# Kernel optimization log

Hardware: AMD Instinct MI355X
Metric: run time of the kernel (lower is better)

Reference implementation:

```python
import jax, jax.numpy as jnp
import numpy as np

HIDDEN = 2048
NUM_HEADS = 16
HEAD_DIM = 128
BLOCK_SIZE = 64
NUM_ACTIVE_BLOCKS = 4  # diagonal pattern -> bandwidth = 2 blocks each side
NEG_INF = -1e30  # stand-in for -inf that is safe under softmax in fp32


def _block_diagonal_additive_mask(seq_len: int) -> jnp.ndarray:
    """Token-level additive mask [S, S]; 0 where block |bi-bj|<=bandwidth, -inf else."""
    bandwidth = NUM_ACTIVE_BLOCKS // 2
    bid = jnp.arange(seq_len) // BLOCK_SIZE  # [S]
    active = jnp.abs(bid[:, None] - bid[None, :]) <= bandwidth  # [S, S] bool
    return jnp.where(active, 0.0, NEG_INF).astype(jnp.float32)


def setup_inputs() -> dict:
    key = jax.random.key(0)
    k0, k1, k2, k3, k4 = jax.random.split(key, 5)
    B, S = 2, 2048
    scale = 1.0 / np.sqrt(HIDDEN)
    return {
        "hidden_states": jax.random.normal(k0, (B, S, HIDDEN), dtype=jnp.float32),
        "Wq": jax.random.normal(k1, (HIDDEN, NUM_HEADS * HEAD_DIM), dtype=jnp.float32) * scale,
        "Wk": jax.random.normal(k2, (HIDDEN, NUM_HEADS * HEAD_DIM), dtype=jnp.float32) * scale,
        "Wv": jax.random.normal(k3, (HIDDEN, NUM_HEADS * HEAD_DIM), dtype=jnp.float32) * scale,
        "Wo": jax.random.normal(k4, (NUM_HEADS * HEAD_DIM, HIDDEN), dtype=jnp.float32) * scale,
    }


def reference(hidden_states, Wq, Wk, Wv, Wo):
    B, S, _ = hidden_states.shape
    scaling = HEAD_DIM ** -0.5

    # projections -> [B, H, S, D]
    def split_heads(x):
        return x.reshape(B, S, NUM_HEADS, HEAD_DIM).transpose(0, 2, 1, 3)

    q = split_heads(hidden_states @ Wq)
    k = split_heads(hidden_states @ Wk)
    v = split_heads(hidden_states @ Wv)

    mask = _block_diagonal_additive_mask(S)  # [S, S]

    # scores [B, H, S, S]
    scores = jnp.einsum("bhsd,bhtd->bhst", q, k) * scaling + mask[None, None]
    attn = jax.nn.softmax(scores.astype(jnp.float32), axis=-1).astype(q.dtype)

    out = jnp.einsum("bhst,bhtd->bhsd", attn, v)  # [B, H, S, D]
    out = out.transpose(0, 2, 1, 3).reshape(B, S, NUM_HEADS * HEAD_DIM)
    return out @ Wo
```

## Files before the change

kernel.cpp:

```cpp
#include <hip/hip_runtime.h>

typedef __attribute__((ext_vector_type(4))) float f32x4;
typedef __attribute__((ext_vector_type(16))) float f32x16;
typedef __attribute__((ext_vector_type(8))) _Float16 f16x8;
typedef __attribute__((ext_vector_type(4))) _Float16 f16x4;

__device__ __forceinline__ void gload_lds16(const void* g, void* l) {
  __builtin_amdgcn_global_load_lds((__attribute__((address_space(1))) void*)(g),
                                   (__attribute__((address_space(3))) void*)(l), 16, 0, 0);
}

#define BAR() asm volatile("s_barrier" ::: "memory")
#define WAITV6() asm volatile("s_waitcnt vmcnt(6)" ::: "memory")
#define WAITV0() asm volatile("s_waitcnt vmcnt(0)" ::: "memory")

__global__ __launch_bounds__(256) void prep(const float* __restrict__ Hs,
                                            const float* __restrict__ W0, const float* __restrict__ W1,
                                            const float* __restrict__ W2, const float* __restrict__ W3,
                                            _Float16* __restrict__ Hb, _Float16* __restrict__ Wt) {
  __shared__ _Float16 tile[64][65];
  const int bid = blockIdx.x, tid = threadIdx.x;
  if (bid < 8192) {
    int i = (bid * 256 + tid) * 4;
    float4 v = *(const float4*)(Hs + i);
    f16x4 o = { (_Float16)v.x, (_Float16)v.y, (_Float16)v.z, (_Float16)v.w };
    *(f16x4*)(Hb + i) = o;
    return;
  }
  const int t = bid - 8192;
  const int z = t >> 10, k0 = ((t >> 5) & 31) * 64, n0 = (t & 31) * 64;
  const float* W = z == 0 ? W0 : z == 1 ? W1 : z == 2 ? W2 : W3;
  _Float16* Wo_ = Wt + (size_t)z * (2048u * 2048u);
  #pragma unroll
  for (int p = 0; p < 4; ++p) {
    int o = p * 256 + tid, r = o >> 4, c = o & 15;
    float4 v = *(const float4*)(W + (size_t)(k0 + r) * 2048 + n0 + c * 4);
    tile[r][c * 4 + 0] = (_Float16)v.x;
    tile[r][c * 4 + 1] = (_Float16)v.y;
    tile[r][c * 4 + 2] = (_Float16)v.z;
    tile[r][c * 4 + 3] = (_Float16)v.w;
  }
  __syncthreads();
  #pragma unroll
  for (int p = 0; p < 2; ++p) {
    int o = p * 256 + tid, nl = o >> 3, c = o & 7;
    f16x8 u;
    #pragma unroll
    for (int i = 0; i < 8; ++i) u[i] = tile[c * 8 + i][nl];
    *(f16x8*)(Wo_ + (size_t)(n0 + nl) * 2048 + k0 + c * 8) = u;
  }
}

template <int SM, int SN, typename OutT>
__device__ __forceinline__ void gemm_tile(const _Float16* __restrict__ A,
                                          const _Float16* __restrict__ Bt,
                                          OutT* __restrict__ C,
                                          int K, int N, int m0, int n0, _Float16* S) {
  _Float16* As = S;
  _Float16* Bs = S + SM * 64 * 64;
  const int tid = threadIdx.x;
  const int lane = tid & 63, w = tid >> 6, l32 = lane & 31, half = lane >> 5;
  const int wm = (w & 1) * SM * 32, wn = (w >> 1) * SN * 32;
  f32x16 acc[SM][SN];
  #pragma unroll
  for (int s = 0; s < SM; ++s)
    #pragma unroll
    for (int t = 0; t < SN; ++t) acc[s][t] = 0;

  for (int k0 = 0; k0 < K; k0 += 64) {
    __syncthreads();
    #pragma unroll
    for (int p = 0; p < SM * 2; ++p) {
      int o = p * 256 + tid, r = o >> 3, c = o & 7;
      gload_lds16(A + (size_t)(m0 + r) * K + k0 + ((c ^ (r & 7)) * 8), (char*)As + o * 16);
    }
    #pragma unroll
    for (int p = 0; p < SN * 2; ++p) {
      int o = p * 256 + tid, r = o >> 3, c = o & 7;
      gload_lds16(Bt + (size_t)(n0 + r) * K + k0 + ((c ^ (r & 7)) * 8), (char*)Bs + o * 16);
    }
    __builtin_amdgcn_s_waitcnt(0);
    __syncthreads();
    #pragma unroll
    for (int kk = 0; kk < 4; ++kk) {
      const int slot = ((2 * kk + half) ^ (l32 & 7)) * 8;
      f16x8 af[SM], bf[SN];
      #pragma unroll
      for (int s = 0; s < SM; ++s) af[s] = *(const f16x8*)(As + (wm + s * 32 + l32) * 64 + slot);
      #pragma unroll
      for (int t = 0; t < SN; ++t) bf[t] = *(const f16x8*)(Bs + (wn + t * 32 + l32) * 64 + slot);
      #pragma unroll
      for (int s = 0; s < SM; ++s)
        #pragma unroll
        for (int t = 0; t < SN; ++t)
          acc[s][t] = __builtin_amdgcn_mfma_f32_32x32x16_f16(bf[t], af[s], acc[s][t], 0, 0, 0);
    }
  }
  #pragma unroll
  for (int s = 0; s < SM; ++s) {
    const size_t row = (size_t)(m0 + wm + s * 32 + l32);
    #pragma unroll
    for (int t = 0; t < SN; ++t) {
      #pragma unroll
      for (int g = 0; g < 4; ++g) {
        const int col = n0 + wn + t * 32 + g * 8 + 4 * half;
        if constexpr (sizeof(OutT) == 2) {
          f16x4 o = { (_Float16)acc[s][t][4 * g + 0], (_Float16)acc[s][t][4 * g + 1],
                      (_Float16)acc[s][t][4 * g + 2], (_Float16)acc[s][t][4 * g + 3] };
          *(f16x4*)((_Float16*)C + row * N + col) = o;
        } else {
          f32x4 o = { acc[s][t][4 * g + 0], acc[s][t][4 * g + 1],
                      acc[s][t][4 * g + 2], acc[s][t][4 * g + 3] };
          *(f32x4*)((float*)C + row * N + col) = o;
        }
      }
    }
  }
}

__device__ __forceinline__ void gemm256(const _Float16* __restrict__ A,
                                        const _Float16* __restrict__ Bt,
                                        _Float16* __restrict__ C, int ldc,
                                        int m0, int n0, _Float16* S) {
  _Float16* const As0 = S;
  _Float16* const As1 = S + 16384;
  _Float16* const Bs0 = S + 32768;
  _Float16* const Bs1 = S + 49152;
  const int tid = (int)threadIdx.x;
  const int lane = tid & 63, w = tid >> 6, l32 = lane & 31, half = lane >> 5;
  const int wm = (w & 1) * 128, wn = (w >> 1) * 64;

  f32x16 acc[4][2];
  #pragma unroll
  for (int s = 0; s < 4; ++s)
    #pragma unroll
    for (int t = 0; t < 2; ++t) acc[s][t] = 0;

  f16x8 af[2][4];
  f16x8 bf[2][4];

  auto stageA = [&](_Float16* dst, int ar, int kt) {
    const int r = tid >> 3, c = tid & 7;
    gload_lds16(A + (size_t)(m0 + ar + r) * 2048 + kt * 64 + ((c ^ (r & 7)) << 3),
                (char*)dst + ar * 128 + tid * 16);
  };
  auto stageB = [&](_Float16* dst, int br, int kt) {
    const int r = tid >> 3, c = tid & 7;
    gload_lds16(Bt + (size_t)(n0 + br + r) * 2048 + kt * 64 + ((c ^ (r & 7)) << 3),
                (char*)dst + br * 128 + tid * 16);
  };
  auto ldA = [&](const _Float16* as, int p) {
    #pragma unroll
    for (int s2 = 0; s2 < 2; ++s2)
      #pragma unroll
      for (int kk = 0; kk < 4; ++kk)
        af[s2][kk] = *(const f16x8*)(as + (wm + p * 64 + s2 * 32 + l32) * 64 +
                                     (((2 * kk + half) ^ (l32 & 7)) << 3));
  };
  auto ldB = [&](const _Float16* bs, int q) {
    #pragma unroll
    for (int kk = 0; kk < 4; ++kk)
      bf[q][kk] = *(const f16x8*)(bs + (wn + q * 32 + l32) * 64 +
                                  (((2 * kk + half) ^ (l32 & 7)) << 3));
  };
  auto mm8 = [&](int sp, int q) {
    __builtin_amdgcn_s_setprio(1);
    #pragma unroll
    for (int kk = 0; kk < 4; ++kk)
      #pragma unroll
      for (int s2 = 0; s2 < 2; ++s2)
        acc[sp * 2 + s2][q] = __builtin_amdgcn_mfma_f32_32x32x16_f16(
            bf[q][kk], af[s2][kk], acc[sp * 2 + s2][q], 0, 0, 0);
    __builtin_amdgcn_s_setprio(0);
  };

  stageA(As0, 0, 0); stageA(As0, 64, 0); stageA(As0, 128, 0); stageA(As0, 192, 0);
  stageB(Bs0, 0, 0); stageB(Bs0, 64, 0); stageB(Bs0, 128, 0); stageB(Bs0, 192, 0);
  stageA(As1, 0, 1); stageA(As1, 128, 1);
  stageB(Bs1, 0, 1); stageB(Bs1, 64, 1); stageB(Bs1, 128, 1); stageB(Bs1, 192, 1);
  WAITV6();
  BAR();

  auto tile = [&](int kt, _Float16* Ac, _Float16* Bc, _Float16* An) {
    const bool g1 = (kt + 1) < 32, g2 = (kt + 2) < 32;
    ldA(Ac, 0);
    ldB(Bc, 0); ldB(Bc, 1);
    if (g1) { stageA(An, 64, kt + 1); stageA(An, 192, kt + 1); }
    mm8(0, 0);
    BAR();
    if (g2) { stageA(Ac, 0, kt + 2); stageA(Ac, 128, kt + 2); }
    mm8(0, 1);
    BAR();
    ldA(Ac, 1);
    if (g2) { stageB(Bc, 0, kt + 2); stageB(Bc, 64, kt + 2);
              stageB(Bc, 128, kt + 2); stageB(Bc, 192, kt + 2); }
    mm8(1, 1);
    mm8(1, 0);
    if (g2) { WAITV6(); } else { WAITV0(); }
    BAR();
  };

  #pragma unroll 1
  for (int kt = 0; kt < 32; kt += 2) {
    tile(kt, As0, Bs0, As1);
    tile(kt + 1, As1, Bs1, As0);
  }

  #pragma unroll
  for (int s = 0; s < 4; ++s) {
    const size_t row = (size_t)(wm + s * 32 + l32);
    #pragma unroll
    for (int t = 0; t < 2; ++t)
      #pragma unroll
      for (int g = 0; g < 4; ++g) {
        const int col = wn + t * 32 + g * 8 + 4 * half;
        f16x4 o = { (_Float16)acc[s][t][4 * g + 0], (_Float16)acc[s][t][4 * g + 1],
                    (_Float16)acc[s][t][4 * g + 2], (_Float16)acc[s][t][4 * g + 3] };
        *(f16x4*)(C + row * ldc + col) = o;
      }
  }
}

__device__ __forceinline__ void gemm128(const _Float16* __restrict__ A,
                                        const _Float16* __restrict__ Bt,
                                        _Float16* __restrict__ C, int ldc,
                                        int m0, int n0, _Float16* S) {
  _Float16* const As0 = S;
  _Float16* const As1 = S + 8192;
  _Float16* const Bs0 = S + 16384;
  _Float16* const Bs1 = S + 32768;
  const int tid = (int)threadIdx.x;
  const int lane = tid & 63, w = tid >> 6, l32 = lane & 31, half = lane >> 5;
  const int wm = (w & 1) * 64, wn = (w >> 1) * 64;

  f32x16 acc[2][2];
  #pragma unroll
  for (int s = 0; s < 2; ++s)
    #pragma unroll
    for (int t = 0; t < 2; ++t) acc[s][t] = 0;

  f16x8 af[2][4], bf[2][4];

  auto stA = [&](_Float16* dst, int ar, int kt) {
    const int r = tid >> 3, c = tid & 7;
    gload_lds16(A + (size_t)(m0 + ar + r) * 2048 + kt * 64 + ((c ^ (r & 7)) << 3),
                (char*)dst + ar * 128 + tid * 16);
  };
  auto stB = [&](_Float16* dst, int br, int kt) {
    const int r = tid >> 3, c = tid & 7;
    gload_lds16(Bt + (size_t)(n0 + br + r) * 2048 + kt * 64 + ((c ^ (r & 7)) << 3),
                (char*)dst + br * 128 + tid * 16);
  };
  auto ldA_ = [&](const _Float16* as) {
    #pragma unroll
    for (int s2 = 0; s2 < 2; ++s2)
      #pragma unroll
      for (int kk = 0; kk < 4; ++kk)
        af[s2][kk] = *(const f16x8*)(as + (wm + s2 * 32 + l32) * 64 +
                                     (((2 * kk + half) ^ (l32 & 7)) << 3));
  };
  auto ldB_ = [&](const _Float16* bs, int q) {
    #pragma unroll
    for (int kk = 0; kk < 4; ++kk)
      bf[q][kk] = *(const f16x8*)(bs + (wn + q * 32 + l32) * 64 +
                                  (((2 * kk + half) ^ (l32 & 7)) << 3));
  };
  auto mmq = [&](int q) {
    __builtin_amdgcn_s_setprio(1);
    #pragma unroll
    for (int kk = 0; kk < 4; ++kk)
      #pragma unroll
      for (int s2 = 0; s2 < 2; ++s2)
        acc[s2][q] = __builtin_amdgcn_mfma_f32_32x32x16_f16(
            bf[q][kk], af[s2][kk], acc[s2][q], 0, 0, 0);
    __builtin_amdgcn_s_setprio(0);
  };

  stA(As0, 0, 0); stA(As0, 64, 0);
  stB(Bs0, 0, 0); stB(Bs0, 64, 0); stB(Bs0, 128, 0); stB(Bs0, 192, 0);
  stA(As1, 0, 1); stA(As1, 64, 1);
  stB(Bs1, 0, 1); stB(Bs1, 64, 1); stB(Bs1, 128, 1); stB(Bs1, 192, 1);
  WAITV6();
  BAR();

  auto tile = [&](int kt, _Float16* Ac, _Float16* Bc) {
    const bool g2 = (kt + 2) < 32;
    ldA_(Ac); ldB_(Bc, 0); ldB_(Bc, 1);
    mmq(0);
    mmq(1);
    BAR();
    if (g2) {
      stA(Ac, 0, kt + 2); stA(Ac, 64, kt + 2);
      stB(Bc, 0, kt + 2); stB(Bc, 64, kt + 2); stB(Bc, 128, kt + 2); stB(Bc, 192, kt + 2);
      WAITV6();
    } else {
      WAITV0();
    }
    BAR();
  };

  #pragma unroll 1
  for (int kt = 0; kt < 32; kt += 2) {
    tile(kt, As0, Bs0);
    tile(kt + 1, As1, Bs1);
  }

  #pragma unroll
  for (int s = 0; s < 2; ++s) {
    const size_t row = (size_t)(wm + s * 32 + l32);
    #pragma unroll
    for (int t = 0; t < 2; ++t)
      #pragma unroll
      for (int g = 0; g < 4; ++g) {
        const int col = wn + t * 32 + g * 8 + 4 * half;
        f16x4 o = { (_Float16)acc[s][t][4 * g + 0], (_Float16)acc[s][t][4 * g + 1],
                    (_Float16)acc[s][t][4 * g + 2], (_Float16)acc[s][t][4 * g + 3] };
        *(f16x4*)(C + row * ldc + col) = o;
      }
  }
}

__global__ __launch_bounds__(512, 2) void qkvv3(const _Float16* __restrict__ Hb,
                                                const _Float16* __restrict__ Wt,
                                                _Float16* __restrict__ Qb,
                                                _Float16* __restrict__ Kb,
                                                _Float16* __restrict__ Vtb) {
  __shared__ _Float16 S[65536];
  const int id = blockIdx.x;
  {
    const int m0 = (id >> 4) * 256, n0 = (id & 15) * 256;
    _Float16* Cq = (n0 < 2048 ? Qb + n0 : Kb + (n0 - 2048)) + (size_t)m0 * 2048;
    gemm256(Hb, Wt, Cq, 2048, m0, n0, S);
  }
  WAITV0();
  BAR();
  {
    const int m0 = (id >> 4) * 128, n0 = (id & 15) * 256;
    gemm128(Wt + (size_t)2 * 4194304, Hb, Vtb + (size_t)m0 * 4096 + n0, 4096, m0, n0, S);
  }
}

__global__ __launch_bounds__(256) void gemm_wo(const _Float16* __restrict__ A,
                                               const _Float16* __restrict__ Bt,
                                               float* __restrict__ C) {
  __shared__ _Float16 S[16384];
  const int t = blockIdx.x;
  gemm_tile<2, 2>(A, Bt, C, 2048, 2048, (t >> 4) * 128, (t & 15) * 128, S);
}

__global__ __launch_bounds__(256) void attn(const _Float16* __restrict__ Qg,
                                            const _Float16* __restrict__ Kg,
                                            const _Float16* __restrict__ Vtg,
                                            _Float16* __restrict__ Og) {
  const int t = blockIdx.x, h = blockIdx.y, b = blockIdx.z;
  __shared__ _Float16 Qs[128 * 128];
  __shared__ _Float16 Ks[64 * 128];
  __shared__ _Float16 Vs[128 * 64];
  const int tid = threadIdx.x;
  const int lane = tid & 63, w = tid >> 6, l16 = lane & 15, quad = lane >> 4;
  const int qbw = 2 * t + (w >> 1);
  const char* QsB = (const char*)Qs;
  const char* KsB = (const char*)Ks;
  const char* VsB = (const char*)Vs;

  #pragma unroll
  for (int p = 0; p < 8; ++p) {
    int o = p * 256 + tid, r = o >> 4, c = o & 15;
    gload_lds16(Qg + (size_t)(b * 2048 + t * 128 + r) * 2048 + h * 128 + ((c ^ (r & 15)) * 8),
                (char*)Qs + o * 16);
  }
  __builtin_amdgcn_s_waitcnt(0);
  __syncthreads();
  f16x8 qf[2][4];
  #pragma unroll
  for (int qc = 0; qc < 2; ++qc)
    #pragma unroll
    for (int ks = 0; ks < 4; ++ks)
      qf[qc][ks] = *(const f16x8*)(QsB + (w * 32 + qc * 16 + l16) * 256 +
                                   (((ks * 4 + quad) ^ l16) * 16));

  const float scale = 0.08838834764831845f;
  float m_[2] = {-1e30f, -1e30f}, l_[2] = {0.f, 0.f};
  f32x4 oacc[8][2];
  #pragma unroll
  for (int dt = 0; dt < 8; ++dt)
    #pragma unroll
    for (int qc = 0; qc < 2; ++qc) oacc[dt][qc] = (f32x4){0.f, 0.f, 0.f, 0.f};

  for (int jj = 0; jj < 6; ++jj) {
    const int j = 2 * t - 2 + jj;
    const int jc = j < 0 ? 0 : (j > 31 ? 31 : j);
    __syncthreads();
    #pragma unroll
    for (int p = 0; p < 4; ++p) {
      int o = p * 256 + tid, r = o >> 4, c = o & 15;
      gload_lds16(Kg + (size_t)(b * 2048 + jc * 64 + r) * 2048 + h * 128 + ((c ^ (r & 15)) * 8),
                  (char*)Ks + o * 16);
    }
    #pragma unroll
    for (int p = 0; p < 4; ++p) {
      int o = p * 256 + tid, d = o >> 3, c = o & 7;
      gload_lds16(Vtg + (size_t)(h * 128 + d) * 4096 + b * 2048 + jc * 64 + ((c ^ (d & 7)) * 8),
                  (char*)Vs + o * 16);
    }
    __builtin_amdgcn_s_waitcnt(0);
    __syncthreads();

    const bool valid = (j >= 0) && (j <= 31) && (j >= qbw - 2) && (j <= qbw + 2);
    if (valid) {
      f32x4 sc[4][2];
      #pragma unroll
      for (int kt = 0; kt < 4; ++kt)
        #pragma unroll
        for (int qc = 0; qc < 2; ++qc) sc[kt][qc] = (f32x4){0.f, 0.f, 0.f, 0.f};
      #pragma unroll
      for (int kt = 0; kt < 4; ++kt)
        #pragma unroll
        for (int ks = 0; ks < 4; ++ks) {
          f16x8 kf = *(const f16x8*)(KsB + (kt * 16 + l16) * 256 + (((ks * 4 + quad) ^ l16) * 16));
          #pragma unroll
          for (int qc = 0; qc < 2; ++qc)
            sc[kt][qc] = __builtin_amdgcn_mfma_f32_16x16x32_f16(kf, qf[qc][ks], sc[kt][qc], 0, 0, 0);
        }
      #pragma unroll
      for (int qc = 0; qc < 2; ++qc) {
        float mj = -1e30f;
        #pragma unroll
        for (int kt = 0; kt < 4; ++kt)
          #pragma unroll
          for (int r = 0; r < 4; ++r) {
            float v = sc[kt][qc][r] * scale;
            sc[kt][qc][r] = v;
            mj = fmaxf(mj, v);
          }
        mj = fmaxf(mj, __shfl_xor(mj, 16));
        mj = fmaxf(mj, __shfl_xor(mj, 32));
        const float mn = fmaxf(m_[qc], mj);
        const float alpha = __expf(m_[qc] - mn);
        float s_ = 0.f;
        #pragma unroll
        for (int kt = 0; kt < 4; ++kt)
          #pragma unroll
          for (int r = 0; r < 4; ++r) {
            float p = __expf(sc[kt][qc][r] - mn);
            sc[kt][qc][r] = p;
            s_ += p;
          }
        s_ += __shfl_xor(s_, 16);
        s_ += __shfl_xor(s_, 32);
        l_[qc] = l_[qc] * alpha + s_;
        m_[qc] = mn;
        #pragma unroll
        for (int dt = 0; dt < 8; ++dt) oacc[dt][qc] *= alpha;
      }
      #pragma unroll
      for (int kt = 0; kt < 4; ++kt) {
        f16x4 pb[2];
        #pragma unroll
        for (int qc = 0; qc < 2; ++qc)
          pb[qc] = (f16x4){ (_Float16)sc[kt][qc][0], (_Float16)sc[kt][qc][1],
                            (_Float16)sc[kt][qc][2], (_Float16)sc[kt][qc][3] };
        #pragma unroll
        for (int dt = 0; dt < 8; ++dt) {
          f16x4 vv = *(const f16x4*)(VsB + (dt * 16 + l16) * 128 +
                                     (((2 * kt + (quad >> 1)) ^ (l16 & 7)) * 16) + (quad & 1) * 8);
          #pragma unroll
          for (int qc = 0; qc < 2; ++qc)
            oacc[dt][qc] = __builtin_amdgcn_mfma_f32_16x16x16f16(vv, pb[qc], oacc[dt][qc], 0, 0, 0);
        }
      }
    }
  }

  #pragma unroll
  for (int qc = 0; qc < 2; ++qc) {
    const float pinv = 1.0f / l_[qc];
    const size_t orow = (size_t)(b * 2048 + t * 128 + w * 32 + qc * 16 + l16);
    #pragma unroll
    for (int dt = 0; dt < 8; ++dt) {
      f16x4 ov = { (_Float16)(oacc[dt][qc][0] * pinv), (_Float16)(oacc[dt][qc][1] * pinv),
                   (_Float16)(oacc[dt][qc][2] * pinv), (_Float16)(oacc[dt][qc][3] * pinv) };
      *(f16x4*)(Og + orow * 2048 + h * 128 + dt * 16 + quad * 4) = ov;
    }
  }
}

extern "C" void kernel_launch(void* const* d_in, const int* in_sizes, int n_in,
                              void* d_out, int out_size, void* d_ws, size_t ws_size,
                              hipStream_t stream) {
  const float* Hs = (const float*)d_in[0];
  const float* Wq = (const float*)d_in[1];
  const float* Wk = (const float*)d_in[2];
  const float* Wv = (const float*)d_in[3];
  const float* Wo = (const float*)d_in[4];
  _Float16* Hb  = (_Float16*)d_ws;
  _Float16* Wt  = Hb  + 8388608;
  _Float16* Qb  = Wt  + 16777216;
  _Float16* Kb  = Qb  + 8388608;
  _Float16* Vtb = Kb  + 8388608;
  _Float16* Ob  = Vtb + 8388608;
  float* out = (float*)d_out;

  prep<<<12288, 256, 0, stream>>>(Hs, Wq, Wk, Wv, Wo, Hb, Wt);
  qkvv3<<<256, 512, 0, stream>>>(Hb, Wt, Qb, Kb, Vtb);
  attn<<<dim3(16, 16, 2), 256, 0, stream>>>(Qb, Kb, Vtb, Ob);
  gemm_wo<<<512, 256, 0, stream>>>(Ob, Wt + (size_t)3 * 4194304, out);
}
```

Measured before the change: 341.0 us.

## Software-pipeline LDS fragment loads in GEMMs and reuse pipelined gemm128 for Wo

Restructures the gemm256 and gemm128 main loops so that register fragments for the next K tile are read from LDS right after the barrier while MFMAs on the current tile proceed. This double-buffers the fragments in registers, which adds register pressure in exchange. The gemm256 loop now stages whole A/B tiles per iteration with adjusted vmcnt waits. The output projection kernel drops the simple unpipelined gemm_tile and uses the templated pipelined gemm128 with 512 threads and 256 blocks, writing float output.

```diff
diff --git a/kernel.cpp b/kernel.cpp
--- a/kernel.cpp
+++ b/kernel.cpp
@@ -11,6 +11,8 @@
 }
 
 #define BAR() asm volatile("s_barrier" ::: "memory")
+#define LGKM0() asm volatile("s_waitcnt lgkmcnt(0)" ::: "memory")
+#define WAITV8() asm volatile("s_waitcnt vmcnt(8)" ::: "memory")
 #define WAITV6() asm volatile("s_waitcnt vmcnt(6)" ::: "memory")
 #define WAITV0() asm volatile("s_waitcnt vmcnt(0)" ::: "memory")
 
@@ -51,73 +53,6 @@
   }
 }
 
-template <int SM, int SN, typename OutT>
-__device__ __forceinline__ void gemm_tile(const _Float16* __restrict__ A,
-                                          const _Float16* __restrict__ Bt,
-                                          OutT* __restrict__ C,
-                                          int K, int N, int m0, int n0, _Float16* S) {
-  _Float16* As = S;
-  _Float16* Bs = S + SM * 64 * 64;
-  const int tid = threadIdx.x;
-  const int lane = tid & 63, w = tid >> 6, l32 = lane & 31, half = lane >> 5;
-  const int wm = (w & 1) * SM * 32, wn = (w >> 1) * SN * 32;
-  f32x16 acc[SM][SN];
-  #pragma unroll
-  for (int s = 0; s < SM; ++s)
-    #pragma unroll
-    for (int t = 0; t < SN; ++t) acc[s][t] = 0;
-
-  for (int k0 = 0; k0 < K; k0 += 64) {
-    __syncthreads();
-    #pragma unroll
-    for (int p = 0; p < SM * 2; ++p) {
-      int o = p * 256 + tid, r = o >> 3, c = o & 7;
-      gload_lds16(A + (size_t)(m0 + r) * K + k0 + ((c ^ (r & 7)) * 8), (char*)As + o * 16);
-    }
-    #pragma unroll
-    for (int p = 0; p < SN * 2; ++p) {
-      int o = p * 256 + tid, r = o >> 3, c = o & 7;
-      gload_lds16(Bt + (size_t)(n0 + r) * K + k0 + ((c ^ (r & 7)) * 8), (char*)Bs + o * 16);
-    }
-    __builtin_amdgcn_s_waitcnt(0);
-    __syncthreads();
-    #pragma unroll
-    for (int kk = 0; kk < 4; ++kk) {
-      const int slot = ((2 * kk + half) ^ (l32 & 7)) * 8;
-      f16x8 af[SM], bf[SN];
-      #pragma unroll
-      for (int s = 0; s < SM; ++s) af[s] = *(const f16x8*)(As + (wm + s * 32 + l32) * 64 + slot);
-      #pragma unroll
-      for (int t = 0; t < SN; ++t) bf[t] = *(const f16x8*)(Bs + (wn + t * 32 + l32) * 64 + slot);
-      #pragma unroll
-      for (int s = 0; s < SM; ++s)
-        #pragma unroll
-        for (int t = 0; t < SN; ++t)
-          acc[s][t] = __builtin_amdgcn_mfma_f32_32x32x16_f16(bf[t], af[s], acc[s][t], 0, 0, 0);
-    }
-  }
-  #pragma unroll
-  for (int s = 0; s < SM; ++s) {
-    const size_t row = (size_t)(m0 + wm + s * 32 + l32);
-    #pragma unroll
-    for (int t = 0; t < SN; ++t) {
-      #pragma unroll
-      for (int g = 0; g < 4; ++g) {
-        const int col = n0 + wn + t * 32 + g * 8 + 4 * half;
-        if constexpr (sizeof(OutT) == 2) {
-          f16x4 o = { (_Float16)acc[s][t][4 * g + 0], (_Float16)acc[s][t][4 * g + 1],
-                      (_Float16)acc[s][t][4 * g + 2], (_Float16)acc[s][t][4 * g + 3] };
-          *(f16x4*)((_Float16*)C + row * N + col) = o;
-        } else {
-          f32x4 o = { acc[s][t][4 * g + 0], acc[s][t][4 * g + 1],
-                      acc[s][t][4 * g + 2], acc[s][t][4 * g + 3] };
-          *(f32x4*)((float*)C + row * N + col) = o;
-        }
-      }
-    }
-  }
-}
-
 __device__ __forceinline__ void gemm256(const _Float16* __restrict__ A,
                                         const _Float16* __restrict__ Bt,
                                         _Float16* __restrict__ C, int ldc,
@@ -136,8 +71,7 @@
     #pragma unroll
     for (int t = 0; t < 2; ++t) acc[s][t] = 0;
 
-  f16x8 af[2][4];
-  f16x8 bf[2][4];
+  f16x8 fA0[2][4], fA1[2][4], fB0[4], fB1[4];
 
   auto stageA = [&](_Float16* dst, int ar, int kt) {
     const int r = tid >> 3, c = tid & 7;
@@ -149,62 +83,68 @@
     gload_lds16(Bt + (size_t)(n0 + br + r) * 2048 + kt * 64 + ((c ^ (r & 7)) << 3),
                 (char*)dst + br * 128 + tid * 16);
   };
-  auto ldA = [&](const _Float16* as, int p) {
+  auto ldA = [&](const _Float16* as, int p, f16x8 (&dst)[2][4]) {
     #pragma unroll
     for (int s2 = 0; s2 < 2; ++s2)
       #pragma unroll
       for (int kk = 0; kk < 4; ++kk)
-        af[s2][kk] = *(const f16x8*)(as + (wm + p * 64 + s2 * 32 + l32) * 64 +
-                                     (((2 * kk + half) ^ (l32 & 7)) << 3));
-  };
-  auto ldB = [&](const _Float16* bs, int q) {
+        dst[s2][kk] = *(const f16x8*)(as + (wm + p * 64 + s2 * 32 + l32) * 64 +
+                                      (((2 * kk + half) ^ (l32 & 7)) << 3));
+  };
+  auto ldB = [&](const _Float16* bs, int q, f16x8 (&dst)[4]) {
     #pragma unroll
     for (int kk = 0; kk < 4; ++kk)
-      bf[q][kk] = *(const f16x8*)(bs + (wn + q * 32 + l32) * 64 +
-                                  (((2 * kk + half) ^ (l32 & 7)) << 3));
-  };
-  auto mm8 = [&](int sp, int q) {
+      dst[kk] = *(const f16x8*)(bs + (wn + q * 32 + l32) * 64 +
+                                (((2 * kk + half) ^ (l32 & 7)) << 3));
+  };
+  auto mmc = [&](const f16x8 (&fa)[2][4], int sp, const f16x8 (&fb)[4], int q) {
     __builtin_amdgcn_s_setprio(1);
     #pragma unroll
     for (int kk = 0; kk < 4; ++kk)
       #pragma unroll
       for (int s2 = 0; s2 < 2; ++s2)
         acc[sp * 2 + s2][q] = __builtin_amdgcn_mfma_f32_32x32x16_f16(
-            bf[q][kk], af[s2][kk], acc[sp * 2 + s2][q], 0, 0, 0);
+            fb[kk], fa[s2][kk], acc[sp * 2 + s2][q], 0, 0, 0);
     __builtin_amdgcn_s_setprio(0);
   };
 
   stageA(As0, 0, 0); stageA(As0, 64, 0); stageA(As0, 128, 0); stageA(As0, 192, 0);
   stageB(Bs0, 0, 0); stageB(Bs0, 64, 0); stageB(Bs0, 128, 0); stageB(Bs0, 192, 0);
-  stageA(As1, 0, 1); stageA(As1, 128, 1);
+  stageA(As1, 0, 1); stageA(As1, 64, 1); stageA(As1, 128, 1); stageA(As1, 192, 1);
   stageB(Bs1, 0, 1); stageB(Bs1, 64, 1); stageB(Bs1, 128, 1); stageB(Bs1, 192, 1);
-  WAITV6();
+  WAITV8();
   BAR();
-
-  auto tile = [&](int kt, _Float16* Ac, _Float16* Bc, _Float16* An) {
-    const bool g1 = (kt + 1) < 32, g2 = (kt + 2) < 32;
-    ldA(Ac, 0);
-    ldB(Bc, 0); ldB(Bc, 1);
-    if (g1) { stageA(An, 64, kt + 1); stageA(An, 192, kt + 1); }
-    mm8(0, 0);
-    BAR();
-    if (g2) { stageA(Ac, 0, kt + 2); stageA(Ac, 128, kt + 2); }
-    mm8(0, 1);
-    BAR();
-    ldA(Ac, 1);
-    if (g2) { stageB(Bc, 0, kt + 2); stageB(Bc, 64, kt + 2);
-              stageB(Bc, 128, kt + 2); stageB(Bc, 192, kt + 2); }
-    mm8(1, 1);
-    mm8(1, 0);
-    if (g2) { WAITV6(); } else { WAITV0(); }
-    BAR();
-  };
+  ldA(As0, 0, fA0);
+  ldB(Bs0, 0, fB0);
+
+#define TILE256(kt, Ac, Bc, An, Bn)                                          \
+  do {                                                                       \
+    const bool g1 = (kt + 1) < 32, g2 = (kt + 2) < 32;                       \
+    ldB(Bc, 1, fB1);                                                         \
+    ldA(Ac, 1, fA1);                                                         \
+    mmc(fA0, 0, fB0, 0);                                                     \
+    mmc(fA0, 0, fB1, 1);                                                     \
+    mmc(fA1, 1, fB0, 0);                                                     \
+    LGKM0();                                                                 \
+    BAR();                      \
+    if (g2) {                                                                \
+      stageA(Ac, 0, kt + 2); stageA(Ac, 64, kt + 2);                         \
+      stageA(Ac, 128, kt + 2); stageA(Ac, 192, kt + 2);                      \
+      stageB(Bc, 0, kt + 2); stageB(Bc, 64, kt + 2);                         \
+      stageB(Bc, 128, kt + 2); stageB(Bc, 192, kt + 2);                      \
+    }                                                                        \
+    if (g2) { WAITV8(); } else { WAITV0(); }                                 \
+    BAR();                           \
+    if (g1) { ldA(An, 0, fA0); ldB(Bn, 0, fB0); }                            \
+    mmc(fA1, 1, fB1, 1);                                                     \
+  } while (0)
 
   #pragma unroll 1
   for (int kt = 0; kt < 32; kt += 2) {
-    tile(kt, As0, Bs0, As1);
-    tile(kt + 1, As1, Bs1, As0);
-  }
+    TILE256(kt, As0, Bs0, As1, Bs1);
+    TILE256(kt + 1, As1, Bs1, As0, Bs0);
+  }
+#undef TILE256
 
   #pragma unroll
   for (int s = 0; s < 4; ++s) {
@@ -221,9 +161,10 @@
   }
 }
 
+template <typename OutT>
 __device__ __forceinline__ void gemm128(const _Float16* __restrict__ A,
                                         const _Float16* __restrict__ Bt,
-                                        _Float16* __restrict__ C, int ldc,
+                                        OutT* __restrict__ C, int ldc,
                                         int m0, int n0, _Float16* S) {
   _Float16* const As0 = S;
   _Float16* const As1 = S + 8192;
@@ -239,7 +180,7 @@
     #pragma unroll
     for (int t = 0; t < 2; ++t) acc[s][t] = 0;
 
-  f16x8 af[2][4], bf[2][4];
+  f16x8 fa[2][4], fan[2][4], fb0[4], fb0n[4], fb1[4];
 
   auto stA = [&](_Float16* dst, int ar, int kt) {
     const int r = tid >> 3, c = tid & 7;
@@ -251,28 +192,28 @@
     gload_lds16(Bt + (size_t)(n0 + br + r) * 2048 + kt * 64 + ((c ^ (r & 7)) << 3),
                 (char*)dst + br * 128 + tid * 16);
   };
-  auto ldA_ = [&](const _Float16* as) {
+  auto ldAq = [&](const _Float16* as, f16x8 (&dst)[2][4]) {
     #pragma unroll
     for (int s2 = 0; s2 < 2; ++s2)
       #pragma unroll
       for (int kk = 0; kk < 4; ++kk)
-        af[s2][kk] = *(const f16x8*)(as + (wm + s2 * 32 + l32) * 64 +
-                                     (((2 * kk + half) ^ (l32 & 7)) << 3));
-  };
-  auto ldB_ = [&](const _Float16* bs, int q) {
+        dst[s2][kk] = *(const f16x8*)(as + (wm + s2 * 32 + l32) * 64 +
+                                      (((2 * kk + half) ^ (l32 & 7)) << 3));
+  };
+  auto ldBq = [&](const _Float16* bs, int q, f16x8 (&dst)[4]) {
     #pragma unroll
     for (int kk = 0; kk < 4; ++kk)
-      bf[q][kk] = *(const f16x8*)(bs + (wn + q * 32 + l32) * 64 +
-                                  (((2 * kk + half) ^ (l32 & 7)) << 3));
-  };
-  auto mmq = [&](int q) {
+      dst[kk] = *(const f16x8*)(bs + (wn + q * 32 + l32) * 64 +
+                                (((2 * kk + half) ^ (l32 & 7)) << 3));
+  };
+  auto mmq = [&](const f16x8 (&fA_)[2][4], const f16x8 (&fB_)[4], int q) {
     __builtin_amdgcn_s_setprio(1);
     #pragma unroll
     for (int kk = 0; kk < 4; ++kk)
       #pragma unroll
       for (int s2 = 0; s2 < 2; ++s2)
         acc[s2][q] = __builtin_amdgcn_mfma_f32_32x32x16_f16(
-            bf[q][kk], af[s2][kk], acc[s2][q], 0, 0, 0);
+            fB_[kk], fA_[s2][kk], acc[s2][q], 0, 0, 0);
     __builtin_amdgcn_s_setprio(0);
   };
 
@@ -282,28 +223,33 @@
   stB(Bs1, 0, 1); stB(Bs1, 64, 1); stB(Bs1, 128, 1); stB(Bs1, 192, 1);
   WAITV6();
   BAR();
-
-  auto tile = [&](int kt, _Float16* Ac, _Float16* Bc) {
-    const bool g2 = (kt + 2) < 32;
-    ldA_(Ac); ldB_(Bc, 0); ldB_(Bc, 1);
-    mmq(0);
-    mmq(1);
-    BAR();
-    if (g2) {
-      stA(Ac, 0, kt + 2); stA(Ac, 64, kt + 2);
-      stB(Bc, 0, kt + 2); stB(Bc, 64, kt + 2); stB(Bc, 128, kt + 2); stB(Bc, 192, kt + 2);
-      WAITV6();
-    } else {
-      WAITV0();
-    }
-    BAR();
-  };
+  ldAq(As0, fa);
+  ldBq(Bs0, 0, fb0);
+
+#define TILE128(kt, Ac, Bc, An, Bn, FA, FB0, FAN, FB0N)                      \
+  do {                                                                       \
+    const bool g1 = (kt + 1) < 32, g2 = (kt + 2) < 32;                       \
+    ldBq(Bc, 1, fb1);                                                        \
+    mmq(FA, FB0, 0);                                                         \
+    LGKM0();                                                                 \
+    BAR();                                                           \
+    if (g2) {                                                                \
+      stA(Ac, 0, kt + 2); stA(Ac, 64, kt + 2);                               \
+      stB(Bc, 0, kt + 2); stB(Bc, 64, kt + 2);                               \
+      stB(Bc, 128, kt + 2); stB(Bc, 192, kt + 2);                            \
+    }                                                                        \
+    if (g2) { WAITV6(); } else { WAITV0(); }                                 \
+    BAR();                                                           \
+    if (g1) { ldAq(An, FAN); ldBq(Bn, 0, FB0N); }                            \
+    mmq(FA, fb1, 1);                                                         \
+  } while (0)
 
   #pragma unroll 1
   for (int kt = 0; kt < 32; kt += 2) {
-    tile(kt, As0, Bs0);
-    tile(kt + 1, As1, Bs1);
-  }
+    TILE128(kt, As0, Bs0, As1, Bs1, fa, fb0, fan, fb0n);
+    TILE128(kt + 1, As1, Bs1, As0, Bs0, fan, fb0n, fa, fb0);
+  }
+#undef TILE128
 
   #pragma unroll
   for (int s = 0; s < 2; ++s) {
@@ -313,9 +259,15 @@
       #pragma unroll
       for (int g = 0; g < 4; ++g) {
         const int col = wn + t * 32 + g * 8 + 4 * half;
-        f16x4 o = { (_Float16)acc[s][t][4 * g + 0], (_Float16)acc[s][t][4 * g + 1],
-                    (_Float16)acc[s][t][4 * g + 2], (_Float16)acc[s][t][4 * g + 3] };
-        *(f16x4*)(C + row * ldc + col) = o;
+        if constexpr (sizeof(OutT) == 2) {
+          f16x4 o = { (_Float16)acc[s][t][4 * g + 0], (_Float16)acc[s][t][4 * g + 1],
+                      (_Float16)acc[s][t][4 * g + 2], (_Float16)acc[s][t][4 * g + 3] };
+          *(f16x4*)((_Float16*)C + row * ldc + col) = o;
+        } else {
+          f32x4 o = { acc[s][t][4 * g + 0], acc[s][t][4 * g + 1],
+                      acc[s][t][4 * g + 2], acc[s][t][4 * g + 3] };
+          *(f32x4*)((float*)C + row * ldc + col) = o;
+        }
       }
   }
 }
@@ -336,16 +288,18 @@
   BAR();
   {
     const int m0 = (id >> 4) * 128, n0 = (id & 15) * 256;
-    gemm128(Wt + (size_t)2 * 4194304, Hb, Vtb + (size_t)m0 * 4096 + n0, 4096, m0, n0, S);
-  }
-}
-
-__global__ __launch_bounds__(256) void gemm_wo(const _Float16* __restrict__ A,
-                                               const _Float16* __restrict__ Bt,
-                                               float* __restrict__ C) {
-  __shared__ _Float16 S[16384];
+    gemm128<_Float16>(Wt + (size_t)2 * 4194304, Hb, Vtb + (size_t)m0 * 4096 + n0,
+                      4096, m0, n0, S);
+  }
+}
+
+__global__ __launch_bounds__(512, 2) void gemm_wo(const _Float16* __restrict__ A,
+                                                  const _Float16* __restrict__ Bt,
+                                                  float* __restrict__ C) {
+  __shared__ _Float16 S[49152];
   const int t = blockIdx.x;
-  gemm_tile<2, 2>(A, Bt, C, 2048, 2048, (t >> 4) * 128, (t & 15) * 128, S);
+  const int m0 = (t >> 3) * 128, n0 = (t & 7) * 256;
+  gemm128<float>(A, Bt, C + (size_t)m0 * 2048 + n0, 2048, m0, n0, S);
 }
 
 __global__ __launch_bounds__(256) void attn(const _Float16* __restrict__ Qg,
@@ -504,5 +458,5 @@
   prep<<<12288, 256, 0, stream>>>(Hs, Wq, Wk, Wv, Wo, Hb, Wt);
   qkvv3<<<256, 512, 0, stream>>>(Hb, Wt, Qb, Kb, Vtb);
   attn<<<dim3(16, 16, 2), 256, 0, stream>>>(Qb, Kb, Vtb, Ob);
-  gemm_wo<<<512, 256, 0, stream>>>(Ob, Wt + (size_t)3 * 4194304, out);
-}
+  gemm_wo<<<256, 512, 0, stream>>>(Ob, Wt + (size_t)3 * 4194304, out);
+}
```

Result: slower. 465.8 us (+36.6%).

## Interleave MFMA phases with barriers and staged loads in QKV GEMMs

Applied to the files above, without the earlier changes.

Restructures the K-loop of the 256-tile and 128-tile GEMMs in the fused QKV kernel. Each MFMA block now sits between sched_barrier-fenced s_barriers, and the LDS fragment reads and global-to-LDS staging are split into smaller chunks placed between compute phases. This is meant to overlap memory traffic with matrix math and keep warps in step. The 128-tile variant also changes the wave-to-column mapping so each wave covers two 32-wide strips 128 apart. The extra barriers add synchronisation cost, and the hard scheduling fences stop the compiler from reordering.

```diff
diff --git a/kernel.cpp b/kernel.cpp
--- a/kernel.cpp
+++ b/kernel.cpp
@@ -10,6 +10,7 @@
                                    (__attribute__((address_space(3))) void*)(l), 16, 0, 0);
 }
 
+#define SB0() __builtin_amdgcn_sched_barrier(0)
 #define BAR() asm volatile("s_barrier" ::: "memory")
 #define WAITV6() asm volatile("s_waitcnt vmcnt(6)" ::: "memory")
 #define WAITV0() asm volatile("s_waitcnt vmcnt(0)" ::: "memory")
@@ -163,7 +164,7 @@
       bf[q][kk] = *(const f16x8*)(bs + (wn + q * 32 + l32) * 64 +
                                   (((2 * kk + half) ^ (l32 & 7)) << 3));
   };
-  auto mm8 = [&](int sp, int q) {
+  auto mm = [&](int sp, int q) {
     __builtin_amdgcn_s_setprio(1);
     #pragma unroll
     for (int kk = 0; kk < 4; ++kk)
@@ -172,6 +173,30 @@
         acc[sp * 2 + s2][q] = __builtin_amdgcn_mfma_f32_32x32x16_f16(
             bf[q][kk], af[s2][kk], acc[sp * 2 + s2][q], 0, 0, 0);
     __builtin_amdgcn_s_setprio(0);
+  };
+
+  auto tile = [&](int kt, _Float16* Ac, _Float16* Bc, _Float16* An) {
+    const bool g1 = (kt + 1) < 32, g2 = (kt + 2) < 32;
+    ldA(Ac, 0); ldB(Bc, 0);
+    if (g1) { stageA(An, 64, kt + 1); stageA(An, 192, kt + 1); }
+    SB0(); BAR(); SB0();
+    mm(0, 0);
+    SB0(); BAR(); SB0();
+    ldB(Bc, 1);
+    if (g2) { stageA(Ac, 0, kt + 2); stageA(Ac, 128, kt + 2); }
+    SB0(); BAR(); SB0();
+    mm(0, 1);
+    SB0(); BAR(); SB0();
+    ldA(Ac, 1);
+    if (g2) { stageB(Bc, 0, kt + 2); stageB(Bc, 64, kt + 2); }
+    SB0(); BAR(); SB0();
+    mm(1, 1);
+    SB0(); BAR(); SB0();
+    if (g2) { stageB(Bc, 128, kt + 2); stageB(Bc, 192, kt + 2); }
+    if (g2) { WAITV6(); } else { WAITV0(); }
+    SB0(); BAR(); SB0();
+    mm(1, 0);
+    SB0(); BAR(); SB0();
   };
 
   stageA(As0, 0, 0); stageA(As0, 64, 0); stageA(As0, 128, 0); stageA(As0, 192, 0);
@@ -179,26 +204,7 @@
   stageA(As1, 0, 1); stageA(As1, 128, 1);
   stageB(Bs1, 0, 1); stageB(Bs1, 64, 1); stageB(Bs1, 128, 1); stageB(Bs1, 192, 1);
   WAITV6();
-  BAR();
-
-  auto tile = [&](int kt, _Float16* Ac, _Float16* Bc, _Float16* An) {
-    const bool g1 = (kt + 1) < 32, g2 = (kt + 2) < 32;
-    ldA(Ac, 0);
-    ldB(Bc, 0); ldB(Bc, 1);
-    if (g1) { stageA(An, 64, kt + 1); stageA(An, 192, kt + 1); }
-    mm8(0, 0);
-    BAR();
-    if (g2) { stageA(Ac, 0, kt + 2); stageA(Ac, 128, kt + 2); }
-    mm8(0, 1);
-    BAR();
-    ldA(Ac, 1);
-    if (g2) { stageB(Bc, 0, kt + 2); stageB(Bc, 64, kt + 2);
-              stageB(Bc, 128, kt + 2); stageB(Bc, 192, kt + 2); }
-    mm8(1, 1);
-    mm8(1, 0);
-    if (g2) { WAITV6(); } else { WAITV0(); }
-    BAR();
-  };
+  SB0(); BAR(); SB0();
 
   #pragma unroll 1
   for (int kt = 0; kt < 32; kt += 2) {
@@ -221,17 +227,17 @@
   }
 }
 
-__device__ __forceinline__ void gemm128(const _Float16* __restrict__ A,
-                                        const _Float16* __restrict__ Bt,
-                                        _Float16* __restrict__ C, int ldc,
-                                        int m0, int n0, _Float16* S) {
+__device__ __forceinline__ void gemm128p(const _Float16* __restrict__ A,
+                                         const _Float16* __restrict__ Bt,
+                                         _Float16* __restrict__ C, int ldc,
+                                         int m0, int n0, _Float16* S) {
   _Float16* const As0 = S;
   _Float16* const As1 = S + 8192;
   _Float16* const Bs0 = S + 16384;
   _Float16* const Bs1 = S + 32768;
   const int tid = (int)threadIdx.x;
   const int lane = tid & 63, w = tid >> 6, l32 = lane & 31, half = lane >> 5;
-  const int wm = (w & 1) * 64, wn = (w >> 1) * 64;
+  const int wm = (w & 1) * 64, wn2 = (w >> 1) * 32;
 
   f32x16 acc[2][2];
   #pragma unroll
@@ -239,7 +245,7 @@
     #pragma unroll
     for (int t = 0; t < 2; ++t) acc[s][t] = 0;
 
-  f16x8 af[2][4], bf[2][4];
+  f16x8 fa[2][4], fb[2][4];
 
   auto stA = [&](_Float16* dst, int ar, int kt) {
     const int r = tid >> 3, c = tid & 7;
@@ -256,13 +262,13 @@
     for (int s2 = 0; s2 < 2; ++s2)
       #pragma unroll
       for (int kk = 0; kk < 4; ++kk)
-        af[s2][kk] = *(const f16x8*)(as + (wm + s2 * 32 + l32) * 64 +
+        fa[s2][kk] = *(const f16x8*)(as + (wm + s2 * 32 + l32) * 64 +
                                      (((2 * kk + half) ^ (l32 & 7)) << 3));
   };
   auto ldB_ = [&](const _Float16* bs, int q) {
     #pragma unroll
     for (int kk = 0; kk < 4; ++kk)
-      bf[q][kk] = *(const f16x8*)(bs + (wn + q * 32 + l32) * 64 +
+      fb[q][kk] = *(const f16x8*)(bs + (q * 128 + wn2 + l32) * 64 +
                                   (((2 * kk + half) ^ (l32 & 7)) << 3));
   };
   auto mmq = [&](int q) {
@@ -272,7 +278,7 @@
       #pragma unroll
       for (int s2 = 0; s2 < 2; ++s2)
         acc[s2][q] = __builtin_amdgcn_mfma_f32_32x32x16_f16(
-            bf[q][kk], af[s2][kk], acc[s2][q], 0, 0, 0);
+            fb[q][kk], fa[s2][kk], acc[s2][q], 0, 0, 0);
     __builtin_amdgcn_s_setprio(0);
   };
 
@@ -281,22 +287,21 @@
   stA(As1, 0, 1); stA(As1, 64, 1);
   stB(Bs1, 0, 1); stB(Bs1, 64, 1); stB(Bs1, 128, 1); stB(Bs1, 192, 1);
   WAITV6();
-  BAR();
+  SB0(); BAR(); SB0();
 
   auto tile = [&](int kt, _Float16* Ac, _Float16* Bc) {
     const bool g2 = (kt + 2) < 32;
-    ldA_(Ac); ldB_(Bc, 0); ldB_(Bc, 1);
+    ldA_(Ac); ldB_(Bc, 0);
     mmq(0);
+    SB0(); BAR(); SB0();
+    ldB_(Bc, 1);
+    if (g2) { stA(Ac, 0, kt + 2); stA(Ac, 64, kt + 2);
+              stB(Bc, 0, kt + 2); stB(Bc, 64, kt + 2); }
     mmq(1);
-    BAR();
-    if (g2) {
-      stA(Ac, 0, kt + 2); stA(Ac, 64, kt + 2);
-      stB(Bc, 0, kt + 2); stB(Bc, 64, kt + 2); stB(Bc, 128, kt + 2); stB(Bc, 192, kt + 2);
-      WAITV6();
-    } else {
-      WAITV0();
-    }
-    BAR();
+    SB0(); BAR(); SB0();
+    if (g2) { stB(Bc, 128, kt + 2); stB(Bc, 192, kt + 2); }
+    if (g2) { WAITV6(); } else { WAITV0(); }
+    SB0(); BAR(); SB0();
   };
 
   #pragma unroll 1
@@ -312,7 +317,7 @@
     for (int t = 0; t < 2; ++t)
       #pragma unroll
       for (int g = 0; g < 4; ++g) {
-        const int col = wn + t * 32 + g * 8 + 4 * half;
+        const int col = t * 128 + wn2 + g * 8 + 4 * half;
         f16x4 o = { (_Float16)acc[s][t][4 * g + 0], (_Float16)acc[s][t][4 * g + 1],
                     (_Float16)acc[s][t][4 * g + 2], (_Float16)acc[s][t][4 * g + 3] };
         *(f16x4*)(C + row * ldc + col) = o;
@@ -333,10 +338,11 @@
     gemm256(Hb, Wt, Cq, 2048, m0, n0, S);
   }
   WAITV0();
-  BAR();
+  SB0(); BAR(); SB0();
   {
     const int m0 = (id >> 4) * 128, n0 = (id & 15) * 256;
-    gemm128(Wt + (size_t)2 * 4194304, Hb, Vtb + (size_t)m0 * 4096 + n0, 4096, m0, n0, S);
+    gemm128p(Wt + (size_t)2 * 4194304, Hb, Vtb + (size_t)m0 * 4096 + n0,
+             4096, m0, n0, S);
   }
 }
 
```

New measurement: 345.7 us. No clear change (+1.4%).

## Use pipelined gemm128 for output projection and split attention K/V waits

Applied to the files above, without the earlier changes.

The output projection now uses the double-buffered gemm128 path (templated for fp32 output) with 512-thread blocks and 128x256 tiles, replacing the simple non-pipelined gemm_tile. This is meant to overlap global-to-LDS loads with MFMA work. In attention, the loop waits only for the K loads (vmcnt 4) before computing scores and softmax, then waits for V before the PV MFMAs, so the V load latency can hide behind the QK work. In exchange it needs more LDS per block and adds a second barrier per iteration.

```diff
diff --git a/kernel.cpp b/kernel.cpp
--- a/kernel.cpp
+++ b/kernel.cpp
@@ -12,6 +12,7 @@
 
 #define BAR() asm volatile("s_barrier" ::: "memory")
 #define WAITV6() asm volatile("s_waitcnt vmcnt(6)" ::: "memory")
+#define WAITV4() asm volatile("s_waitcnt vmcnt(4)" ::: "memory")
 #define WAITV0() asm volatile("s_waitcnt vmcnt(0)" ::: "memory")
 
 __global__ __launch_bounds__(256) void prep(const float* __restrict__ Hs,
@@ -51,73 +52,6 @@
   }
 }
 
-template <int SM, int SN, typename OutT>
-__device__ __forceinline__ void gemm_tile(const _Float16* __restrict__ A,
-                                          const _Float16* __restrict__ Bt,
-                                          OutT* __restrict__ C,
-                                          int K, int N, int m0, int n0, _Float16* S) {
-  _Float16* As = S;
-  _Float16* Bs = S + SM * 64 * 64;
-  const int tid = threadIdx.x;
-  const int lane = tid & 63, w = tid >> 6, l32 = lane & 31, half = lane >> 5;
-  const int wm = (w & 1) * SM * 32, wn = (w >> 1) * SN * 32;
-  f32x16 acc[SM][SN];
-  #pragma unroll
-  for (int s = 0; s < SM; ++s)
-    #pragma unroll
-    for (int t = 0; t < SN; ++t) acc[s][t] = 0;
-
-  for (int k0 = 0; k0 < K; k0 += 64) {
-    __syncthreads();
-    #pragma unroll
-    for (int p = 0; p < SM * 2; ++p) {
-      int o = p * 256 + tid, r = o >> 3, c = o & 7;
-      gload_lds16(A + (size_t)(m0 + r) * K + k0 + ((c ^ (r & 7)) * 8), (char*)As + o * 16);
-    }
-    #pragma unroll
-    for (int p = 0; p < SN * 2; ++p) {
-      int o = p * 256 + tid, r = o >> 3, c = o & 7;
-      gload_lds16(Bt + (size_t)(n0 + r) * K + k0 + ((c ^ (r & 7)) * 8), (char*)Bs + o * 16);
-    }
-    __builtin_amdgcn_s_waitcnt(0);
-    __syncthreads();
-    #pragma unroll
-    for (int kk = 0; kk < 4; ++kk) {
-      const int slot = ((2 * kk + half) ^ (l32 & 7)) * 8;
-      f16x8 af[SM], bf[SN];
-      #pragma unroll
-      for (int s = 0; s < SM; ++s) af[s] = *(const f16x8*)(As + (wm + s * 32 + l32) * 64 + slot);
-      #pragma unroll
-      for (int t = 0; t < SN; ++t) bf[t] = *(const f16x8*)(Bs + (wn + t * 32 + l32) * 64 + slot);
-      #pragma unroll
-      for (int s = 0; s < SM; ++s)
-        #pragma unroll
-        for (int t = 0; t < SN; ++t)
-          acc[s][t] = __builtin_amdgcn_mfma_f32_32x32x16_f16(bf[t], af[s], acc[s][t], 0, 0, 0);
-    }
-  }
-  #pragma unroll
-  for (int s = 0; s < SM; ++s) {
-    const size_t row = (size_t)(m0 + wm + s * 32 + l32);
-    #pragma unroll
-    for (int t = 0; t < SN; ++t) {
-      #pragma unroll
-      for (int g = 0; g < 4; ++g) {
-        const int col = n0 + wn + t * 32 + g * 8 + 4 * half;
-        if constexpr (sizeof(OutT) == 2) {
-          f16x4 o = { (_Float16)acc[s][t][4 * g + 0], (_Float16)acc[s][t][4 * g + 1],
-                      (_Float16)acc[s][t][4 * g + 2], (_Float16)acc[s][t][4 * g + 3] };
-          *(f16x4*)((_Float16*)C + row * N + col) = o;
-        } else {
-          f32x4 o = { acc[s][t][4 * g + 0], acc[s][t][4 * g + 1],
-                      acc[s][t][4 * g + 2], acc[s][t][4 * g + 3] };
-          *(f32x4*)((float*)C + row * N + col) = o;
-        }
-      }
-    }
-  }
-}
-
 __device__ __forceinline__ void gemm256(const _Float16* __restrict__ A,
                                         const _Float16* __restrict__ Bt,
                                         _Float16* __restrict__ C, int ldc,
@@ -221,9 +155,10 @@
   }
 }
 
+template <typename OutT>
 __device__ __forceinline__ void gemm128(const _Float16* __restrict__ A,
                                         const _Float16* __restrict__ Bt,
-                                        _Float16* __restrict__ C, int ldc,
+                                        OutT* __restrict__ C, int ldc,
                                         int m0, int n0, _Float16* S) {
   _Float16* const As0 = S;
   _Float16* const As1 = S + 8192;
@@ -251,7 +186,7 @@
     gload_lds16(Bt + (size_t)(n0 + br + r) * 2048 + kt * 64 + ((c ^ (r & 7)) << 3),
                 (char*)dst + br * 128 + tid * 16);
   };
-  auto ldA_ = [&](const _Float16* as) {
+  auto ldAq = [&](const _Float16* as) {
     #pragma unroll
     for (int s2 = 0; s2 < 2; ++s2)
       #pragma unroll
@@ -259,7 +194,7 @@
         af[s2][kk] = *(const f16x8*)(as + (wm + s2 * 32 + l32) * 64 +
                                      (((2 * kk + half) ^ (l32 & 7)) << 3));
   };
-  auto ldB_ = [&](const _Float16* bs, int q) {
+  auto ldBq = [&](const _Float16* bs, int q) {
     #pragma unroll
     for (int kk = 0; kk < 4; ++kk)
       bf[q][kk] = *(const f16x8*)(bs + (wn + q * 32 + l32) * 64 +
@@ -285,7 +220,7 @@
 
   auto tile = [&](int kt, _Float16* Ac, _Float16* Bc) {
     const bool g2 = (kt + 2) < 32;
-    ldA_(Ac); ldB_(Bc, 0); ldB_(Bc, 1);
+    ldAq(Ac); ldBq(Bc, 0); ldBq(Bc, 1);
     mmq(0);
     mmq(1);
     BAR();
@@ -313,9 +248,15 @@
       #pragma unroll
       for (int g = 0; g < 4; ++g) {
         const int col = wn + t * 32 + g * 8 + 4 * half;
-        f16x4 o = { (_Float16)acc[s][t][4 * g + 0], (_Float16)acc[s][t][4 * g + 1],
-                    (_Float16)acc[s][t][4 * g + 2], (_Float16)acc[s][t][4 * g + 3] };
-        *(f16x4*)(C + row * ldc + col) = o;
+        if constexpr (sizeof(OutT) == 2) {
+          f16x4 o = { (_Float16)acc[s][t][4 * g + 0], (_Float16)acc[s][t][4 * g + 1],
+                      (_Float16)acc[s][t][4 * g + 2], (_Float16)acc[s][t][4 * g + 3] };
+          *(f16x4*)((_Float16*)C + row * ldc + col) = o;
+        } else {
+          f32x4 o = { acc[s][t][4 * g + 0], acc[s][t][4 * g + 1],
+                      acc[s][t][4 * g + 2], acc[s][t][4 * g + 3] };
+          *(f32x4*)((float*)C + row * ldc + col) = o;
+        }
       }
   }
 }
@@ -336,16 +277,18 @@
   BAR();
   {
     const int m0 = (id >> 4) * 128, n0 = (id & 15) * 256;
-    gemm128(Wt + (size_t)2 * 4194304, Hb, Vtb + (size_t)m0 * 4096 + n0, 4096, m0, n0, S);
-  }
-}
-
-__global__ __launch_bounds__(256) void gemm_wo(const _Float16* __restrict__ A,
-                                               const _Float16* __restrict__ Bt,
-                                               float* __restrict__ C) {
-  __shared__ _Float16 S[16384];
+    gemm128<_Float16>(Wt + (size_t)2 * 4194304, Hb, Vtb + (size_t)m0 * 4096 + n0,
+                      4096, m0, n0, S);
+  }
+}
+
+__global__ __launch_bounds__(512, 2) void gemm_wo(const _Float16* __restrict__ A,
+                                                  const _Float16* __restrict__ Bt,
+                                                  float* __restrict__ C) {
+  __shared__ _Float16 S[49152];
   const int t = blockIdx.x;
-  gemm_tile<2, 2>(A, Bt, C, 2048, 2048, (t >> 4) * 128, (t & 15) * 128, S);
+  const int m0 = (t >> 3) * 128, n0 = (t & 7) * 256;
+  gemm128<float>(A, Bt, C + (size_t)m0 * 2048 + n0, 2048, m0, n0, S);
 }
 
 __global__ __launch_bounds__(256) void attn(const _Float16* __restrict__ Qg,
@@ -403,12 +346,13 @@
       gload_lds16(Vtg + (size_t)(h * 128 + d) * 4096 + b * 2048 + jc * 64 + ((c ^ (d & 7)) * 8),
                   (char*)Vs + o * 16);
     }
-    __builtin_amdgcn_s_waitcnt(0);
-    __syncthreads();
+    WAITV4();
+    BAR();
 
     const bool valid = (j >= 0) && (j <= 31) && (j >= qbw - 2) && (j <= qbw + 2);
+    f32x4 sc[4][2];
+    f16x4 pb[4][2];
     if (valid) {
-      f32x4 sc[4][2];
       #pragma unroll
       for (int kt = 0; kt < 4; ++kt)
         #pragma unroll
@@ -454,19 +398,24 @@
         for (int dt = 0; dt < 8; ++dt) oacc[dt][qc] *= alpha;
       }
       #pragma unroll
+      for (int kt = 0; kt < 4; ++kt)
+        #pragma unroll
+        for (int qc = 0; qc < 2; ++qc)
+          pb[kt][qc] = (f16x4){ (_Float16)sc[kt][qc][0], (_Float16)sc[kt][qc][1],
+                                (_Float16)sc[kt][qc][2], (_Float16)sc[kt][qc][3] };
+    }
+    WAITV0();
+    BAR();
+    if (valid) {
+      #pragma unroll
       for (int kt = 0; kt < 4; ++kt) {
-        f16x4 pb[2];
-        #pragma unroll
-        for (int qc = 0; qc < 2; ++qc)
-          pb[qc] = (f16x4){ (_Float16)sc[kt][qc][0], (_Float16)sc[kt][qc][1],
-                            (_Float16)sc[kt][qc][2], (_Float16)sc[kt][qc][3] };
         #pragma unroll
         for (int dt = 0; dt < 8; ++dt) {
           f16x4 vv = *(const f16x4*)(VsB + (dt * 16 + l16) * 128 +
                                      (((2 * kt + (quad >> 1)) ^ (l16 & 7)) * 16) + (quad & 1) * 8);
           #pragma unroll
           for (int qc = 0; qc < 2; ++qc)
-            oacc[dt][qc] = __builtin_amdgcn_mfma_f32_16x16x16f16(vv, pb[qc], oacc[dt][qc], 0, 0, 0);
+            oacc[dt][qc] = __builtin_amdgcn_mfma_f32_16x16x16f16(vv, pb[kt][qc], oacc[dt][qc], 0, 0, 0);
         }
       }
     }
@@ -504,5 +453,5 @@
   prep<<<12288, 256, 0, stream>>>(Hs, Wq, Wk, Wv, Wo, Hb, Wt);
   qkvv3<<<256, 512, 0, stream>>>(Hb, Wt, Qb, Kb, Vtb);
   attn<<<dim3(16, 16, 2), 256, 0, stream>>>(Qb, Kb, Vtb, Ob);
-  gemm_wo<<<512, 256, 0, stream>>>(Ob, Wt + (size_t)3 * 4194304, out);
-}
+  gemm_wo<<<256, 512, 0, stream>>>(Ob, Wt + (size_t)3 * 4194304, out);
+}
```

After: 341.4 us. About the same (+0.1%).
